# Kernel tuning notes

Measured on AMD Instinct MI355X. Metric: run time of the kernel, lower is better.

## Reference

```python
import jax, jax.numpy as jnp
import numpy as np

B, S, D, H = 2, 2048, 1024, 16
HD = D // H  # head_dim = 64
ROPE_BASE = 10000.0
NEG_MIN = jnp.finfo(jnp.float32).min


def _rope_cos_sin(seq_len, head_dim):
    inv_freq = 1.0 / (ROPE_BASE ** (jnp.arange(0, head_dim, 2, dtype=jnp.float32) / head_dim))
    t = jnp.arange(seq_len, dtype=jnp.float32)
    freqs = jnp.einsum('i,j->ij', t, inv_freq)           # [S, HD/2]
    emb = jnp.concatenate([freqs, freqs], axis=-1)        # [S, HD]
    return jnp.cos(emb), jnp.sin(emb)


def _rotate_half(x):
    x1, x2 = jnp.split(x, 2, axis=-1)
    return jnp.concatenate([-x2, x1], axis=-1)


def setup_inputs() -> dict:
    key = jax.random.key(0)
    ks = jax.random.split(key, 5)
    sc = 0.02
    hidden_states = jax.random.normal(ks[0], (B, S, D), dtype=jnp.float32)
    wq = jax.random.normal(ks[1], (D, D), dtype=jnp.float32) * sc
    wk = jax.random.normal(ks[2], (D, D), dtype=jnp.float32) * sc
    wv = jax.random.normal(ks[3], (D, D), dtype=jnp.float32) * sc
    wo = jax.random.normal(ks[4], (D, D), dtype=jnp.float32) * sc
    # additive causal mask [B,1,S,S]: 0 on/below diagonal, large negative above
    causal = jnp.tril(jnp.ones((S, S), dtype=jnp.bool_))
    attention_mask = jnp.where(causal, 0.0, NEG_MIN)[None, None, :, :].astype(jnp.float32)
    attention_mask = jnp.broadcast_to(attention_mask, (B, 1, S, S))
    position_ids = jnp.broadcast_to(jnp.arange(S, dtype=jnp.int32)[None, :], (B, S))
    return {"hidden_states": hidden_states, "attention_mask": attention_mask,
            "wq": wq, "wk": wk, "wv": wv, "wo": wo, "position_ids": position_ids}


def reference(hidden_states, attention_mask, wq, wk, wv, wo, position_ids):
    bsz, q_len, _ = hidden_states.shape

    def shape_heads(x):
        return x.reshape(bsz, q_len, H, HD).transpose(0, 2, 1, 3)  # [B,H,S,HD]

    q = shape_heads(hidden_states @ wq)
    k = shape_heads(hidden_states @ wk)
    v = shape_heads(hidden_states @ wv)

    cos, sin = _rope_cos_sin(q_len, HD)                   # [S, HD]
    cos = cos[position_ids][:, None, :, :]                # [B,1,S,HD]
    sin = sin[position_ids][:, None, :, :]
    q = q * cos + _rotate_half(q) * sin
    k = k * cos + _rotate_half(k) * sin

    scores = jnp.einsum('bhqd,bhkd->bhqk', q, k) / jnp.sqrt(jnp.float32(HD))
    scores = jnp.maximum(scores + attention_mask, NEG_MIN)
    attn = jax.nn.softmax(scores, axis=-1)
    out = jnp.einsum('bhqk,bhkd->bhqd', attn, v)          # [B,H,S,HD]
    out = out.transpose(0, 2, 1, 3).reshape(bsz, q_len, D)
    return out @ wo
```

## Files before the change

kernel.cpp:

```cpp
#include <hip/hip_runtime.h>
#include <hip/hip_bf16.h>

#define B_ 2
#define S_ 2048
#define D_ 1024
#define H_ 16
#define HD_ 64

typedef unsigned short u16;
typedef __attribute__((ext_vector_type(8))) short short8;
typedef __attribute__((ext_vector_type(4))) float f32x4;

#if __has_builtin(__builtin_amdgcn_exp2f)
#define EXP2F(x) __builtin_amdgcn_exp2f(x)
#else
#define EXP2F(x) exp2f(x)
#endif

__device__ __forceinline__ u16 f2bf(float f) {
  union { float f; unsigned u; } v; v.f = f;
  unsigned r = v.u + 0x7fffu + ((v.u >> 16) & 1u);
  return (u16)(r >> 16);
}
__device__ __forceinline__ unsigned pkbf(float a, float b) {
  union { __hip_bfloat162 h; unsigned u; } v;
  v.h = __float22bfloat162_rn(float2{a, b});
  return v.u;
}
__device__ __forceinline__ void gload_lds16(const u16* g, u16* l) {
  __builtin_amdgcn_global_load_lds((const __attribute__((address_space(1))) void*)g,
                                   (__attribute__((address_space(3))) void*)l, 16, 0, 0);
}

__global__ __launch_bounds__(256) void prep_kernel(const float* __restrict__ hs,
                                                   const float* __restrict__ W0,
                                                   const float* __restrict__ W1,
                                                   const float* __restrict__ W2,
                                                   const float* __restrict__ W3,
                                                   u16* __restrict__ Xb,
                                                   u16* __restrict__ WT) {
  __shared__ float T[64][65];
  if (blockIdx.z == 4) {
    const int base = (blockIdx.y * 16 + blockIdx.x) * 4096 + threadIdx.x;
#pragma unroll 4
    for (int i = 0; i < 16; ++i) {
      const int idx = base + i * 256;
      const float4 v = ((const float4*)hs)[idx];
      ushort4 o;
      o.x = f2bf(v.x); o.y = f2bf(v.y); o.z = f2bf(v.z); o.w = f2bf(v.w);
      ((ushort4*)Xb)[idx] = o;
    }
    return;
  }
  const float* Wz[4] = {W0, W1, W2, W3};
  const float* W = Wz[blockIdx.z];
  u16* dst = WT + (size_t)blockIdx.z * (1024 * 1024);
  const int nb = blockIdx.x * 64, kb = blockIdx.y * 64;
  const int t = threadIdx.x;
  const int r = t >> 2, c4 = (t & 3) * 16;
#pragma unroll
  for (int i = 0; i < 4; ++i) {
    float4 v = *(const float4*)&W[(kb + r) * D_ + nb + c4 + i * 4];
    T[r][c4 + i * 4 + 0] = v.x;
    T[r][c4 + i * 4 + 1] = v.y;
    T[r][c4 + i * 4 + 2] = v.z;
    T[r][c4 + i * 4 + 3] = v.w;
  }
  __syncthreads();
#pragma unroll
  for (int i = 0; i < 4; ++i) {
    ushort4 o;
    o.x = f2bf(T[c4 + i * 4 + 0][r]);
    o.y = f2bf(T[c4 + i * 4 + 1][r]);
    o.z = f2bf(T[c4 + i * 4 + 2][r]);
    o.w = f2bf(T[c4 + i * 4 + 3][r]);
    *(ushort4*)&dst[(nb + r) * D_ + kb + c4 + i * 4] = o;
  }
}

template <int BN, int MODE>
__global__ __launch_bounds__(256) void gemm_kernel(const u16* __restrict__ A,
                                                   const u16* __restrict__ BT,
                                                   float* __restrict__ out0,
                                                   u16* __restrict__ oQ,
                                                   u16* __restrict__ oK,
                                                   u16* __restrict__ oV,
                                                   const int* __restrict__ posarr) {
  constexpr int K = D_;
  constexpr int BK = 32;
  constexpr int NSTEP = K / BK;
  constexpr int NT = BN / 32;
  constexpr int NBR = (BN * BK) / 2048;
  constexpr int ABANK = 128 * BK;
  constexpr int BBANK = BN * BK;
  constexpr int BUFSZ = ABANK + BBANK;
  constexpr int EPIU = (MODE == 1) ? 128 * 136 : 0;
  constexpr int SMU = (3 * BUFSZ > EPIU) ? 3 * BUFSZ : EPIU;
  __shared__ u16 smem[SMU];

  const int t = threadIdx.x, lane = t & 63, w = t >> 6;
  const int l15 = lane & 15, quad = lane >> 4;
  const int flat = blockIdx.x;
  const int xcd = flat & 7, j = flat >> 3;
  const int m0 = ((xcd << 2) + (j & 3)) * 128;
  const int n0 = (j >> 2) * BN;
  const int wm = (w >> 1) * 64, wn = (w & 1) * (BN / 2);

  f32x4 acc[4][NT];
#pragma unroll
  for (int mt = 0; mt < 4; ++mt)
#pragma unroll
    for (int nt = 0; nt < NT; ++nt) acc[mt][nt] = (f32x4){0.f, 0.f, 0.f, 0.f};

  const u16* agp[2]; int adst[2];
  const u16* bgp[NBR]; int bdst[NBR];
#pragma unroll
  for (int jj = 0; jj < 2; ++jj) {
    const int slot = jj * 256 + w * 64 + lane;
    const int row = slot >> 2, c = slot & 3, q = c ^ ((row >> 1) & 3);
    agp[jj] = A + (size_t)(m0 + row) * K + q * 8;
    adst[jj] = (jj * 256 + w * 64) * 8;
  }
#pragma unroll
  for (int jj = 0; jj < NBR; ++jj) {
    const int slot = jj * 256 + w * 64 + lane;
    const int row = slot >> 2, c = slot & 3, q = c ^ ((row >> 1) & 3);
    bgp[jj] = BT + (size_t)(n0 + row) * K + q * 8;
    bdst[jj] = ABANK + (jj * 256 + w * 64) * 8;
  }

  auto stage = [&](int k0, int buf) {
    u16* base = smem + buf * BUFSZ;
#pragma unroll
    for (int jj = 0; jj < 2; ++jj) gload_lds16(agp[jj] + k0, base + adst[jj]);
#pragma unroll
    for (int jj = 0; jj < NBR; ++jj) gload_lds16(bgp[jj] + k0, base + bdst[jj]);
  };

  int afo[4], bfo[NT];
#pragma unroll
  for (int mt = 0; mt < 4; ++mt) {
    const int row = wm + mt * 16 + l15;
    afo[mt] = row * BK + (quad ^ ((row >> 1) & 3)) * 8;
  }
#pragma unroll
  for (int nt = 0; nt < NT; ++nt) {
    const int col = wn + nt * 16 + l15;
    bfo[nt] = ABANK + col * BK + (quad ^ ((col >> 1) & 3)) * 8;
  }

  auto compute = [&](int buf) {
    const u16* base = smem + buf * BUFSZ;
    short8 af[4], bf[NT];
#pragma unroll
    for (int mt = 0; mt < 4; ++mt) af[mt] = *(const short8*)&base[afo[mt]];
#pragma unroll
    for (int nt = 0; nt < NT; ++nt) bf[nt] = *(const short8*)&base[bfo[nt]];
#pragma unroll
    for (int mt = 0; mt < 4; ++mt)
#pragma unroll
      for (int nt = 0; nt < NT; ++nt)
        acc[mt][nt] = __builtin_amdgcn_mfma_f32_16x16x32_bf16(af[mt], bf[nt], acc[mt][nt], 0, 0, 0);
  };

  stage(0, 0);
  stage(BK, 1);
  int bc = 0, bs = 2;
#pragma unroll 1
  for (int it = 0; it < NSTEP - 2; ++it) {
    if constexpr (MODE == 1) asm volatile("s_waitcnt vmcnt(4)" ::: "memory");
    else                     asm volatile("s_waitcnt vmcnt(3)" ::: "memory");
    __builtin_amdgcn_s_barrier();
    __builtin_amdgcn_sched_barrier(0);
    stage((it + 2) * BK, bs);
    compute(bc);
    bc = bc == 2 ? 0 : bc + 1;
    bs = bs == 2 ? 0 : bs + 1;
  }
  if constexpr (MODE == 1) asm volatile("s_waitcnt vmcnt(4)" ::: "memory");
  else                     asm volatile("s_waitcnt vmcnt(3)" ::: "memory");
  __builtin_amdgcn_s_barrier();
  __builtin_amdgcn_sched_barrier(0);
  compute(bc);
  bc = bc == 2 ? 0 : bc + 1;
  asm volatile("s_waitcnt vmcnt(0)" ::: "memory");
  __builtin_amdgcn_s_barrier();
  __builtin_amdgcn_sched_barrier(0);
  compute(bc);

  if (MODE == 0) {
#pragma unroll
    for (int mt = 0; mt < 4; ++mt) {
      const int row0 = m0 + wm + mt * 16 + quad * 4;
#pragma unroll
      for (int nt = 0; nt < NT; ++nt) {
        const int col = n0 + wn + nt * 16 + l15;
#pragma unroll
        for (int r = 0; r < 4; ++r) out0[(size_t)(row0 + r) * 1024 + col] = acc[mt][nt][r];
      }
    }
  } else {
    const int widx = n0 >> 10;
    if (widx == 2) {
      __syncthreads();
      u16* Epi = smem;
#pragma unroll
      for (int nt = 0; nt < NT; ++nt) {
        const int col = wn + nt * 16 + l15;
#pragma unroll
        for (int mt = 0; mt < 4; ++mt) {
          const int row0 = wm + mt * 16 + quad * 4;
          uint2 pk;
          pk.x = pkbf(acc[mt][nt][0], acc[mt][nt][1]);
          pk.y = pkbf(acc[mt][nt][2], acc[mt][nt][3]);
          *(uint2*)&Epi[col * 136 + row0] = pk;
        }
      }
      __syncthreads();
      const int col = t >> 1, half = t & 1;
      const int cc = (n0 + col) & 1023;
      const int h = cc >> 6, d = cc & 63;
      const int bb = m0 >> 11;
      const int s0 = (m0 & (S_ - 1)) + half * 64;
      u16* gp = oV + ((((size_t)(bb * H_ + h) * HD_ + d)) << 11) + s0;
#pragma unroll
      for (int i = 0; i < 8; ++i)
        ((uint4*)gp)[i] = *(const uint4*)&Epi[col * 136 + half * 64 + i * 8];
    } else {
      u16* dst = (widx == 0) ? oQ : oK;
      const float scale = (widx == 0) ? 0.18033688011f : 1.0f;
      float invf[2];
      invf[0] = exp2f(-0.41524101186f * (float)l15);
      invf[1] = exp2f(-0.41524101186f * (float)(16 + l15));
      __syncthreads();
      u16* Epi = smem;
#pragma unroll
      for (int mt = 0; mt < 4; ++mt) {
        const int lrow0 = wm + mt * 16 + quad * 4;
#pragma unroll
        for (int r = 0; r < 4; ++r) {
          const int rw = m0 + lrow0 + r;
          const int b = rw >> 11, s = rw & (S_ - 1);
          const float pos = (float)posarr[b * S_ + s];
#pragma unroll
          for (int nt2 = 0; nt2 < 2; ++nt2) {
            float sn, c;
            __sincosf(pos * invf[nt2], &sn, &c);
            const float x1 = acc[mt][nt2][r], x2 = acc[mt][nt2 + 2][r];
            const int d = nt2 * 16 + l15;
            Epi[(lrow0 + r) * 136 + wn + d] = f2bf((x1 * c - x2 * sn) * scale);
            Epi[(lrow0 + r) * 136 + wn + d + 32] = f2bf((x2 * c + x1 * sn) * scale);
          }
        }
      }
      __syncthreads();
      const int bb = m0 >> 11, s0 = m0 & (S_ - 1);
      const int sl = t >> 1, d0 = (t & 1) * 32;
#pragma unroll
      for (int hh = 0; hh < 2; ++hh) {
        const int h = ((n0 + hh * 64) & 1023) >> 6;
        u16* gp = dst + (((size_t)(bb * H_ + h) * S_ + s0 + sl) << 6) + d0;
#pragma unroll
        for (int k2 = 0; k2 < 4; ++k2)
          ((uint4*)gp)[k2] = *(const uint4*)&Epi[sl * 136 + hh * 64 + d0 + k2 * 8];
      }
    }
  }
}

__global__ __launch_bounds__(256, 2) void attn_kernel(const u16* __restrict__ Q,
                                                      const u16* __restrict__ Kx,
                                                      const u16* __restrict__ Vt,
                                                      u16* __restrict__ AO) {
  __shared__ u16 Ks[2][2][512 * 8];
  __shared__ u16 Vs[2][2][512 * 8];
  __shared__ u16 Pw[4][128 * 8];
  const int t = threadIdx.x;
  const int lane = t & 63, w = t >> 6;
  const int l15 = lane & 15, quad = lane >> 4;
  const int idx = blockIdx.x;
  const int pr = (idx >> 3) & 15;
  const int bh = (idx & 7) | ((idx >> 7) << 3);
  const int qtA = pr, qtB = 31 - pr;
  const u16* qp = Q + bh * (S_ * HD_);
  const u16* kp = Kx + bh * (S_ * HD_);
  const u16* vp = Vt + bh * (HD_ * S_);
  const int wq16 = w * 16;
  const int q_loA = qtA * 64 + wq16;
  const int q_loB = qtB * 64 + wq16;

  int srow[2], sq[2];
#pragma unroll
  for (int jj = 0; jj < 2; ++jj) {
    int slot = w * 128 + jj * 64 + lane;
    srow[jj] = slot >> 3;
    sq[jj] = (slot & 7) ^ (srow[jj] & 7);
  }
  auto stageT = [&](int kt, int buf, int tt) {
#pragma unroll
    for (int jj = 0; jj < 2; ++jj)
      gload_lds16(kp + (size_t)(kt * 64 + srow[jj]) * 64 + sq[jj] * 8,
                  &Ks[buf][tt][(w * 128 + jj * 64) * 8]);
#pragma unroll
    for (int jj = 0; jj < 2; ++jj)
      gload_lds16(vp + (size_t)srow[jj] * S_ + kt * 64 + sq[jj] * 8,
                  &Vs[buf][tt][(w * 128 + jj * 64) * 8]);
  };
  auto stageGroup = [&](int g, int buf, int ktmax) {
    const int kt0 = g * 2;
    stageT(kt0, buf, 0);
    if (kt0 + 1 <= ktmax) stageT(kt0 + 1, buf, 1);
  };

  short8 qfA[2], qfB[2];
#pragma unroll
  for (int kc = 0; kc < 2; ++kc) {
    qfA[kc] = *(const short8*)&qp[(q_loA + l15) * HD_ + kc * 32 + quad * 8];
    qfB[kc] = *(const short8*)&qp[(q_loB + l15) * HD_ + kc * 32 + quad * 8];
  }

  f32x4 oA[4], oB[4];
  float mA = -INFINITY, lA = 0.f, mB = -INFINITY, lB = 0.f;
#pragma unroll
  for (int i = 0; i < 4; ++i) {
    oA[i] = (f32x4){0.f, 0.f, 0.f, 0.f};
    oB[i] = (f32x4){0.f, 0.f, 0.f, 0.f};
  }

  auto chainStep = [&](bool diag, const short8* qf, const short8* kf, const short8* vf,
                       f32x4* o, float& m_, float& l_) {
    f32x4 sa[4];
#pragma unroll
    for (int i = 0; i < 4; ++i) sa[i] = (f32x4){0.f, 0.f, 0.f, 0.f};
#pragma unroll
    for (int kc = 0; kc < 2; ++kc)
#pragma unroll
      for (int nt = 0; nt < 4; ++nt)
        sa[nt] = __builtin_amdgcn_mfma_f32_16x16x32_bf16(kf[kc * 4 + nt], qf[kc], sa[nt], 0, 0, 0);
    if (diag) {
#pragma unroll
      for (int nt = 0; nt < 4; ++nt)
#pragma unroll
        for (int r = 0; r < 4; ++r)
          if (nt * 16 + quad * 4 + r > wq16 + l15) sa[nt][r] = -INFINITY;
    }
    float mx = -INFINITY;
#pragma unroll
    for (int nt = 0; nt < 4; ++nt)
#pragma unroll
      for (int r = 0; r < 4; ++r) mx = fmaxf(mx, sa[nt][r]);
    mx = fmaxf(mx, __shfl_xor(mx, 16));
    mx = fmaxf(mx, __shfl_xor(mx, 32));
    const float mn = fmaxf(m_, mx);
    const float alpha = EXP2F(m_ - mn);
    m_ = mn;
    float p[16];
    float sum = 0.f;
#pragma unroll
    for (int nt = 0; nt < 4; ++nt)
#pragma unroll
      for (int r = 0; r < 4; ++r) {
        const float pe = EXP2F(sa[nt][r] - mn);
        p[nt * 4 + r] = pe;
        sum += pe;
      }
    sum += __shfl_xor(sum, 16);
    sum += __shfl_xor(sum, 32);
    l_ = l_ * alpha + sum;
#pragma unroll
    for (int dt = 0; dt < 4; ++dt)
#pragma unroll
      for (int r = 0; r < 4; ++r) o[dt][r] *= alpha;
#pragma unroll
    for (int nt = 0; nt < 4; ++nt) {
      const int q = nt * 2 + (quad >> 1);
      uint2 pk;
      pk.x = pkbf(p[nt * 4 + 0], p[nt * 4 + 1]);
      pk.y = pkbf(p[nt * 4 + 2], p[nt * 4 + 3]);
      *(uint2*)&Pw[w][(l15 * 8 + (q ^ (l15 & 7))) * 8 + (quad & 1) * 4] = pk;
    }
#pragma unroll
    for (int kc = 0; kc < 2; ++kc) {
      short8 pf = *(const short8*)&Pw[w][(l15 * 8 + (((kc * 4) + quad) ^ (l15 & 7))) * 8];
#pragma unroll
      for (int dt = 0; dt < 4; ++dt)
        o[dt] = __builtin_amdgcn_mfma_f32_16x16x32_bf16(vf[dt * 2 + kc], pf, o[dt], 0, 0, 0);
    }
  };

  auto loadFrags = [&](int buf, int tt, short8* kf, short8* vf) {
#pragma unroll
    for (int kc = 0; kc < 2; ++kc)
#pragma unroll
      for (int nt = 0; nt < 4; ++nt) {
        const int row = nt * 16 + l15;
        kf[kc * 4 + nt] =
            *(const short8*)&Ks[buf][tt][(row * 8 + ((kc * 4 + quad) ^ (row & 7))) * 8];
      }
#pragma unroll
    for (int dt = 0; dt < 4; ++dt)
#pragma unroll
      for (int kc = 0; kc < 2; ++kc) {
        const int row = dt * 16 + l15;
        vf[dt * 2 + kc] =
            *(const short8*)&Vs[buf][tt][(row * 8 + ((kc * 4 + quad) ^ (row & 7))) * 8];
      }
  };

  const int ktmax = qtB;
  const int ngroups = (ktmax + 2) >> 1;
  short8 kf[8], vf[8];
  stageGroup(0, 0, ktmax);
#pragma unroll 1
  for (int g = 0; g < ngroups; ++g) {
    __syncthreads();
    if (g + 1 < ngroups) stageGroup(g + 1, (g + 1) & 1, ktmax);
    const int buf = g & 1;
    const int kt0 = 2 * g;
    loadFrags(buf, 0, kf, vf);
    chainStep(kt0 == qtB, qfB, kf, vf, oB, mB, lB);
    if (kt0 <= qtA) chainStep(kt0 == qtA, qfA, kf, vf, oA, mA, lA);
    if (kt0 + 1 <= ktmax) {
      loadFrags(buf, 1, kf, vf);
      chainStep(kt0 + 1 == qtB, qfB, kf, vf, oB, mB, lB);
      if (kt0 + 1 <= qtA) chainStep(kt0 + 1 == qtA, qfA, kf, vf, oA, mA, lA);
    }
  }

  const int b = bh >> 4, h = bh & 15;
  const float liA = 1.0f / lA, liB = 1.0f / lB;
  const size_t baseA = ((size_t)(b * S_ + q_loA + l15)) * D_ + h * HD_;
  const size_t baseB = ((size_t)(b * S_ + q_loB + l15)) * D_ + h * HD_;
#pragma unroll
  for (int dt = 0; dt < 4; ++dt)
#pragma unroll
    for (int rr = 0; rr < 2; ++rr) {
      *(unsigned*)&AO[baseA + dt * 16 + quad * 4 + rr * 2] =
          pkbf(oA[dt][rr * 2] * liA, oA[dt][rr * 2 + 1] * liA);
      *(unsigned*)&AO[baseB + dt * 16 + quad * 4 + rr * 2] =
          pkbf(oB[dt][rr * 2] * liB, oB[dt][rr * 2 + 1] * liB);
    }
}

extern "C" void kernel_launch(void* const* d_in, const int* in_sizes, int n_in,
                              void* d_out, int out_size, void* d_ws, size_t ws_size,
                              hipStream_t stream) {
  const float* hs = (const float*)d_in[0];
  const float* wq = (const float*)d_in[2];
  const float* wk = (const float*)d_in[3];
  const float* wv = (const float*)d_in[4];
  const float* wo = (const float*)d_in[5];
  const int* pos = (const int*)d_in[6];
  float* out = (float*)d_out;

  char* ws = (char*)d_ws;
  const size_t MB = (size_t)1 << 20;
  u16* Xb = (u16*)(ws);
  u16* WT = (u16*)(ws + 8 * MB);
  u16* Qh = (u16*)(ws + 16 * MB);
  u16* Kh = (u16*)(ws + 24 * MB);
  u16* Vt = (u16*)(ws + 32 * MB);
  u16* AO = (u16*)(ws + 40 * MB);

  prep_kernel<<<dim3(16, 16, 5), 256, 0, stream>>>(hs, wq, wk, wv, wo, Xb, WT);

  gemm_kernel<128, 1><<<768, 256, 0, stream>>>(Xb, WT, nullptr, Qh, Kh, Vt, pos);

  attn_kernel<<<512, 256, 0, stream>>>(Qh, Kh, Vt, AO);

  gemm_kernel<64, 0><<<512, 256, 0, stream>>>(AO, WT + 3 * 1024 * 1024, out,
                                              nullptr, nullptr, nullptr, nullptr);
}
```

Measured before the change: 201.1 us.

## Split attention blocks to one query tile each with row sums via MFMA

Each attention block used to process a paired short and long query tile. It now handles a single query tile, so the grid doubles to 1024 blocks, LDS staging is single-tile double-buffered, and launch bounds allow 4 blocks per CU for higher occupancy. The softmax row sum is now accumulated with an extra MFMA against a ones vector instead of shuffles. Rescaling is skipped when the running max does not change, and setprio hints are placed around the MFMA sections. In exchange, each K/V tile is no longer reused by two query tiles, which raises global and LDS traffic per unit of work, and an interleaved long/short tile ordering is relied on to balance the causal workload.

After: 222.7 us. +10.7%, slower.

```diff
diff --git a/kernel.cpp b/kernel.cpp
--- a/kernel.cpp
+++ b/kernel.cpp
@@ -268,26 +268,26 @@
   }
 }
 
-__global__ __launch_bounds__(256, 2) void attn_kernel(const u16* __restrict__ Q,
+__global__ __launch_bounds__(256, 4) void attn_kernel(const u16* __restrict__ Q,
                                                       const u16* __restrict__ Kx,
                                                       const u16* __restrict__ Vt,
                                                       u16* __restrict__ AO) {
-  __shared__ u16 Ks[2][2][512 * 8];
-  __shared__ u16 Vs[2][2][512 * 8];
+  __shared__ u16 Ks[2][512 * 8];
+  __shared__ u16 Vs[2][512 * 8];
   __shared__ u16 Pw[4][128 * 8];
   const int t = threadIdx.x;
   const int lane = t & 63, w = t >> 6;
   const int l15 = lane & 15, quad = lane >> 4;
   const int idx = blockIdx.x;
-  const int pr = (idx >> 3) & 15;
-  const int bh = (idx & 7) | ((idx >> 7) << 3);
-  const int qtA = pr, qtB = 31 - pr;
+  const int r = idx >> 3;
+  const int j = r & 31;
+  const int qt = (j & 1) ? (j >> 1) : (31 - (j >> 1));
+  const int bh = (idx & 7) | ((r >> 5) << 3);
   const u16* qp = Q + bh * (S_ * HD_);
   const u16* kp = Kx + bh * (S_ * HD_);
   const u16* vp = Vt + bh * (HD_ * S_);
   const int wq16 = w * 16;
-  const int q_loA = qtA * 64 + wq16;
-  const int q_loB = qtB * 64 + wq16;
+  const int q_lo = qt * 64 + wq16;
 
   int srow[2], sq[2];
 #pragma unroll
@@ -296,81 +296,96 @@
     srow[jj] = slot >> 3;
     sq[jj] = (slot & 7) ^ (srow[jj] & 7);
   }
-  auto stageT = [&](int kt, int buf, int tt) {
+  auto stage = [&](int kt, int buf) {
 #pragma unroll
     for (int jj = 0; jj < 2; ++jj)
       gload_lds16(kp + (size_t)(kt * 64 + srow[jj]) * 64 + sq[jj] * 8,
-                  &Ks[buf][tt][(w * 128 + jj * 64) * 8]);
+                  &Ks[buf][(w * 128 + jj * 64) * 8]);
 #pragma unroll
     for (int jj = 0; jj < 2; ++jj)
       gload_lds16(vp + (size_t)srow[jj] * S_ + kt * 64 + sq[jj] * 8,
-                  &Vs[buf][tt][(w * 128 + jj * 64) * 8]);
+                  &Vs[buf][(w * 128 + jj * 64) * 8]);
   };
-  auto stageGroup = [&](int g, int buf, int ktmax) {
-    const int kt0 = g * 2;
-    stageT(kt0, buf, 0);
-    if (kt0 + 1 <= ktmax) stageT(kt0 + 1, buf, 1);
-  };
-
-  short8 qfA[2], qfB[2];
-#pragma unroll
-  for (int kc = 0; kc < 2; ++kc) {
-    qfA[kc] = *(const short8*)&qp[(q_loA + l15) * HD_ + kc * 32 + quad * 8];
-    qfB[kc] = *(const short8*)&qp[(q_loB + l15) * HD_ + kc * 32 + quad * 8];
-  }
-
-  f32x4 oA[4], oB[4];
-  float mA = -INFINITY, lA = 0.f, mB = -INFINITY, lB = 0.f;
-#pragma unroll
-  for (int i = 0; i < 4; ++i) {
-    oA[i] = (f32x4){0.f, 0.f, 0.f, 0.f};
-    oB[i] = (f32x4){0.f, 0.f, 0.f, 0.f};
-  }
-
-  auto chainStep = [&](bool diag, const short8* qf, const short8* kf, const short8* vf,
-                       f32x4* o, float& m_, float& l_) {
+
+  short8 qf[2];
+#pragma unroll
+  for (int kc = 0; kc < 2; ++kc)
+    qf[kc] = *(const short8*)&qp[(q_lo + l15) * HD_ + kc * 32 + quad * 8];
+
+  f32x4 o[4];
+  f32x4 lsum = (f32x4){0.f, 0.f, 0.f, 0.f};
+  float m_ = -INFINITY;
+#pragma unroll
+  for (int i = 0; i < 4; ++i) o[i] = (f32x4){0.f, 0.f, 0.f, 0.f};
+  const short8 ones = {0x3F80, 0x3F80, 0x3F80, 0x3F80, 0x3F80, 0x3F80, 0x3F80, 0x3F80};
+
+  stage(0, 0);
+#pragma unroll 1
+  for (int kt = 0; kt <= qt; ++kt) {
+    __syncthreads();
+    if (kt < qt) stage(kt + 1, (kt + 1) & 1);
+    const int buf = kt & 1;
+
+    short8 kf[8];
+#pragma unroll
+    for (int kc = 0; kc < 2; ++kc)
+#pragma unroll
+      for (int nt = 0; nt < 4; ++nt) {
+        const int row = nt * 16 + l15;
+        kf[kc * 4 + nt] =
+            *(const short8*)&Ks[buf][(row * 8 + ((kc * 4 + quad) ^ (row & 7))) * 8];
+      }
     f32x4 sa[4];
 #pragma unroll
     for (int i = 0; i < 4; ++i) sa[i] = (f32x4){0.f, 0.f, 0.f, 0.f};
+    __builtin_amdgcn_s_setprio(1);
 #pragma unroll
     for (int kc = 0; kc < 2; ++kc)
 #pragma unroll
       for (int nt = 0; nt < 4; ++nt)
         sa[nt] = __builtin_amdgcn_mfma_f32_16x16x32_bf16(kf[kc * 4 + nt], qf[kc], sa[nt], 0, 0, 0);
-    if (diag) {
+    __builtin_amdgcn_s_setprio(0);
+
+    short8 vf[8];
+#pragma unroll
+    for (int dt = 0; dt < 4; ++dt)
+#pragma unroll
+      for (int kc = 0; kc < 2; ++kc) {
+        const int row = dt * 16 + l15;
+        vf[dt * 2 + kc] =
+            *(const short8*)&Vs[buf][(row * 8 + ((kc * 4 + quad) ^ (row & 7))) * 8];
+      }
+
+    if (kt == qt) {
 #pragma unroll
       for (int nt = 0; nt < 4; ++nt)
 #pragma unroll
-        for (int r = 0; r < 4; ++r)
-          if (nt * 16 + quad * 4 + r > wq16 + l15) sa[nt][r] = -INFINITY;
-    }
-    float mx = -INFINITY;
+        for (int rr = 0; rr < 4; ++rr)
+          if (nt * 16 + quad * 4 + rr > wq16 + l15) sa[nt][rr] = -INFINITY;
+    }
+    float mq[4];
 #pragma unroll
     for (int nt = 0; nt < 4; ++nt)
-#pragma unroll
-      for (int r = 0; r < 4; ++r) mx = fmaxf(mx, sa[nt][r]);
+      mq[nt] = fmaxf(fmaxf(sa[nt][0], sa[nt][1]), fmaxf(sa[nt][2], sa[nt][3]));
+    float mx = fmaxf(fmaxf(mq[0], mq[1]), fmaxf(mq[2], mq[3]));
     mx = fmaxf(mx, __shfl_xor(mx, 16));
     mx = fmaxf(mx, __shfl_xor(mx, 32));
-    const float mn = fmaxf(m_, mx);
-    const float alpha = EXP2F(m_ - mn);
-    m_ = mn;
+    if (!__all(mx <= m_)) {
+      const float mn = fmaxf(m_, mx);
+      const float alpha = EXP2F(m_ - mn);
+      m_ = mn;
+#pragma unroll
+      for (int dt = 0; dt < 4; ++dt)
+#pragma unroll
+        for (int rr = 0; rr < 4; ++rr) o[dt][rr] *= alpha;
+#pragma unroll
+      for (int rr = 0; rr < 4; ++rr) lsum[rr] *= alpha;
+    }
     float p[16];
-    float sum = 0.f;
 #pragma unroll
     for (int nt = 0; nt < 4; ++nt)
 #pragma unroll
-      for (int r = 0; r < 4; ++r) {
-        const float pe = EXP2F(sa[nt][r] - mn);
-        p[nt * 4 + r] = pe;
-        sum += pe;
-      }
-    sum += __shfl_xor(sum, 16);
-    sum += __shfl_xor(sum, 32);
-    l_ = l_ * alpha + sum;
-#pragma unroll
-    for (int dt = 0; dt < 4; ++dt)
-#pragma unroll
-      for (int r = 0; r < 4; ++r) o[dt][r] *= alpha;
+      for (int rr = 0; rr < 4; ++rr) p[nt * 4 + rr] = EXP2F(sa[nt][rr] - m_);
 #pragma unroll
     for (int nt = 0; nt < 4; ++nt) {
       const int q = nt * 2 + (quad >> 1);
@@ -379,67 +394,27 @@
       pk.y = pkbf(p[nt * 4 + 2], p[nt * 4 + 3]);
       *(uint2*)&Pw[w][(l15 * 8 + (q ^ (l15 & 7))) * 8 + (quad & 1) * 4] = pk;
     }
+    __builtin_amdgcn_s_setprio(1);
 #pragma unroll
     for (int kc = 0; kc < 2; ++kc) {
       short8 pf = *(const short8*)&Pw[w][(l15 * 8 + (((kc * 4) + quad) ^ (l15 & 7))) * 8];
 #pragma unroll
       for (int dt = 0; dt < 4; ++dt)
         o[dt] = __builtin_amdgcn_mfma_f32_16x16x32_bf16(vf[dt * 2 + kc], pf, o[dt], 0, 0, 0);
-    }
-  };
-
-  auto loadFrags = [&](int buf, int tt, short8* kf, short8* vf) {
-#pragma unroll
-    for (int kc = 0; kc < 2; ++kc)
-#pragma unroll
-      for (int nt = 0; nt < 4; ++nt) {
-        const int row = nt * 16 + l15;
-        kf[kc * 4 + nt] =
-            *(const short8*)&Ks[buf][tt][(row * 8 + ((kc * 4 + quad) ^ (row & 7))) * 8];
-      }
-#pragma unroll
-    for (int dt = 0; dt < 4; ++dt)
-#pragma unroll
-      for (int kc = 0; kc < 2; ++kc) {
-        const int row = dt * 16 + l15;
-        vf[dt * 2 + kc] =
-            *(const short8*)&Vs[buf][tt][(row * 8 + ((kc * 4 + quad) ^ (row & 7))) * 8];
-      }
-  };
-
-  const int ktmax = qtB;
-  const int ngroups = (ktmax + 2) >> 1;
-  short8 kf[8], vf[8];
-  stageGroup(0, 0, ktmax);
-#pragma unroll 1
-  for (int g = 0; g < ngroups; ++g) {
-    __syncthreads();
-    if (g + 1 < ngroups) stageGroup(g + 1, (g + 1) & 1, ktmax);
-    const int buf = g & 1;
-    const int kt0 = 2 * g;
-    loadFrags(buf, 0, kf, vf);
-    chainStep(kt0 == qtB, qfB, kf, vf, oB, mB, lB);
-    if (kt0 <= qtA) chainStep(kt0 == qtA, qfA, kf, vf, oA, mA, lA);
-    if (kt0 + 1 <= ktmax) {
-      loadFrags(buf, 1, kf, vf);
-      chainStep(kt0 + 1 == qtB, qfB, kf, vf, oB, mB, lB);
-      if (kt0 + 1 <= qtA) chainStep(kt0 + 1 == qtA, qfA, kf, vf, oA, mA, lA);
-    }
+      lsum = __builtin_amdgcn_mfma_f32_16x16x32_bf16(ones, pf, lsum, 0, 0, 0);
+    }
+    __builtin_amdgcn_s_setprio(0);
   }
 
   const int b = bh >> 4, h = bh & 15;
-  const float liA = 1.0f / lA, liB = 1.0f / lB;
-  const size_t baseA = ((size_t)(b * S_ + q_loA + l15)) * D_ + h * HD_;
-  const size_t baseB = ((size_t)(b * S_ + q_loB + l15)) * D_ + h * HD_;
+  const float li = 1.0f / lsum[0];
+  const size_t base = ((size_t)(b * S_ + q_lo + l15)) * D_ + h * HD_;
 #pragma unroll
   for (int dt = 0; dt < 4; ++dt)
 #pragma unroll
-    for (int rr = 0; rr < 2; ++rr) {
-      *(unsigned*)&AO[baseA + dt * 16 + quad * 4 + rr * 2] =
-          pkbf(oA[dt][rr * 2] * liA, oA[dt][rr * 2 + 1] * liA);
-      *(unsigned*)&AO[baseB + dt * 16 + quad * 4 + rr * 2] =
-          pkbf(oB[dt][rr * 2] * liB, oB[dt][rr * 2 + 1] * liB);
-    }
+    for (int rr = 0; rr < 2; ++rr)
+      *(unsigned*)&AO[base + dt * 16 + quad * 4 + rr * 2] =
+          pkbf(o[dt][rr * 2] * li, o[dt][rr * 2 + 1] * li);
 }
 
 extern "C" void kernel_launch(void* const* d_in, const int* in_sizes, int n_in,
@@ -466,7 +441,7 @@
 
   gemm_kernel<128, 1><<<768, 256, 0, stream>>>(Xb, WT, nullptr, Qh, Kh, Vt, pos);
 
-  attn_kernel<<<512, 256, 0, stream>>>(Qh, Kh, Vt, AO);
+  attn_kernel<<<1024, 256, 0, stream>>>(Qh, Kh, Vt, AO);
 
   gemm_kernel<64, 0><<<512, 256, 0, stream>>>(AO, WT + 3 * 1024 * 1024, out,
                                               nullptr, nullptr, nullptr, nullptr);
```

## Compute softmax row sums via MFMA, skip rescale when max unchanged, add setprio

Applied to the files above, without the earlier changes.

Replaces the per-lane row-sum reduction with an extra MFMA against a ones vector, so the row sum comes from the same bf16 P values used for the PV product. The alpha rescale of the accumulators is skipped when no lane's running max increases. The QK and PV MFMA blocks are wrapped in s_setprio, and the P scratch buffer is split per chain (A/B) so the two chains can overlap in LDS. It removes VALU work and shuffles from the softmax path but adds two MFMAs per step and a wave-wide vote branch.

Measured after the change: 203.4 us. About the same (+1.1%).

```diff
diff --git a/kernel.cpp b/kernel.cpp
--- a/kernel.cpp
+++ b/kernel.cpp
@@ -274,7 +274,7 @@
                                                       u16* __restrict__ AO) {
   __shared__ u16 Ks[2][2][512 * 8];
   __shared__ u16 Vs[2][2][512 * 8];
-  __shared__ u16 Pw[4][128 * 8];
+  __shared__ u16 Pw[4][2][128 * 8];
   const int t = threadIdx.x;
   const int lane = t & 63, w = t >> 6;
   const int l15 = lane & 15, quad = lane >> 4;
@@ -320,23 +320,27 @@
   }
 
   f32x4 oA[4], oB[4];
-  float mA = -INFINITY, lA = 0.f, mB = -INFINITY, lB = 0.f;
+  f32x4 lsA = (f32x4){0.f, 0.f, 0.f, 0.f}, lsB = (f32x4){0.f, 0.f, 0.f, 0.f};
+  float mA = -INFINITY, mB = -INFINITY;
 #pragma unroll
   for (int i = 0; i < 4; ++i) {
     oA[i] = (f32x4){0.f, 0.f, 0.f, 0.f};
     oB[i] = (f32x4){0.f, 0.f, 0.f, 0.f};
   }
+  const short8 ones = {0x3F80, 0x3F80, 0x3F80, 0x3F80, 0x3F80, 0x3F80, 0x3F80, 0x3F80};
 
   auto chainStep = [&](bool diag, const short8* qf, const short8* kf, const short8* vf,
-                       f32x4* o, float& m_, float& l_) {
+                       f32x4* o, float& m_, f32x4& ls, u16* pwb) {
     f32x4 sa[4];
 #pragma unroll
     for (int i = 0; i < 4; ++i) sa[i] = (f32x4){0.f, 0.f, 0.f, 0.f};
+    __builtin_amdgcn_s_setprio(1);
 #pragma unroll
     for (int kc = 0; kc < 2; ++kc)
 #pragma unroll
       for (int nt = 0; nt < 4; ++nt)
         sa[nt] = __builtin_amdgcn_mfma_f32_16x16x32_bf16(kf[kc * 4 + nt], qf[kc], sa[nt], 0, 0, 0);
+    __builtin_amdgcn_s_setprio(0);
     if (diag) {
 #pragma unroll
       for (int nt = 0; nt < 4; ++nt)
@@ -344,48 +348,41 @@
         for (int r = 0; r < 4; ++r)
           if (nt * 16 + quad * 4 + r > wq16 + l15) sa[nt][r] = -INFINITY;
     }
-    float mx = -INFINITY;
+    float mq[4];
 #pragma unroll
     for (int nt = 0; nt < 4; ++nt)
-#pragma unroll
-      for (int r = 0; r < 4; ++r) mx = fmaxf(mx, sa[nt][r]);
+      mq[nt] = fmaxf(fmaxf(sa[nt][0], sa[nt][1]), fmaxf(sa[nt][2], sa[nt][3]));
+    float mx = fmaxf(fmaxf(mq[0], mq[1]), fmaxf(mq[2], mq[3]));
     mx = fmaxf(mx, __shfl_xor(mx, 16));
     mx = fmaxf(mx, __shfl_xor(mx, 32));
-    const float mn = fmaxf(m_, mx);
-    const float alpha = EXP2F(m_ - mn);
-    m_ = mn;
-    float p[16];
-    float sum = 0.f;
-#pragma unroll
-    for (int nt = 0; nt < 4; ++nt)
-#pragma unroll
-      for (int r = 0; r < 4; ++r) {
-        const float pe = EXP2F(sa[nt][r] - mn);
-        p[nt * 4 + r] = pe;
-        sum += pe;
-      }
-    sum += __shfl_xor(sum, 16);
-    sum += __shfl_xor(sum, 32);
-    l_ = l_ * alpha + sum;
-#pragma unroll
-    for (int dt = 0; dt < 4; ++dt)
-#pragma unroll
-      for (int r = 0; r < 4; ++r) o[dt][r] *= alpha;
+    if (!__all(mx <= m_)) {
+      const float mn = fmaxf(m_, mx);
+      const float alpha = EXP2F(m_ - mn);
+      m_ = mn;
+#pragma unroll
+      for (int dt = 0; dt < 4; ++dt)
+#pragma unroll
+        for (int r = 0; r < 4; ++r) o[dt][r] *= alpha;
+      ls *= alpha;
+    }
 #pragma unroll
     for (int nt = 0; nt < 4; ++nt) {
       const int q = nt * 2 + (quad >> 1);
       uint2 pk;
-      pk.x = pkbf(p[nt * 4 + 0], p[nt * 4 + 1]);
-      pk.y = pkbf(p[nt * 4 + 2], p[nt * 4 + 3]);
-      *(uint2*)&Pw[w][(l15 * 8 + (q ^ (l15 & 7))) * 8 + (quad & 1) * 4] = pk;
-    }
+      pk.x = pkbf(EXP2F(sa[nt][0] - m_), EXP2F(sa[nt][1] - m_));
+      pk.y = pkbf(EXP2F(sa[nt][2] - m_), EXP2F(sa[nt][3] - m_));
+      *(uint2*)&pwb[(l15 * 8 + (q ^ (l15 & 7))) * 8 + (quad & 1) * 4] = pk;
+    }
+    __builtin_amdgcn_s_setprio(1);
 #pragma unroll
     for (int kc = 0; kc < 2; ++kc) {
-      short8 pf = *(const short8*)&Pw[w][(l15 * 8 + (((kc * 4) + quad) ^ (l15 & 7))) * 8];
+      short8 pf = *(const short8*)&pwb[(l15 * 8 + (((kc * 4) + quad) ^ (l15 & 7))) * 8];
 #pragma unroll
       for (int dt = 0; dt < 4; ++dt)
         o[dt] = __builtin_amdgcn_mfma_f32_16x16x32_bf16(vf[dt * 2 + kc], pf, o[dt], 0, 0, 0);
-    }
+      ls = __builtin_amdgcn_mfma_f32_16x16x32_bf16(ones, pf, ls, 0, 0, 0);
+    }
+    __builtin_amdgcn_s_setprio(0);
   };
 
   auto loadFrags = [&](int buf, int tt, short8* kf, short8* vf) {
@@ -418,17 +415,17 @@
     const int buf = g & 1;
     const int kt0 = 2 * g;
     loadFrags(buf, 0, kf, vf);
-    chainStep(kt0 == qtB, qfB, kf, vf, oB, mB, lB);
-    if (kt0 <= qtA) chainStep(kt0 == qtA, qfA, kf, vf, oA, mA, lA);
+    chainStep(kt0 == qtB, qfB, kf, vf, oB, mB, lsB, &Pw[w][1][0]);
+    if (kt0 <= qtA) chainStep(kt0 == qtA, qfA, kf, vf, oA, mA, lsA, &Pw[w][0][0]);
     if (kt0 + 1 <= ktmax) {
       loadFrags(buf, 1, kf, vf);
-      chainStep(kt0 + 1 == qtB, qfB, kf, vf, oB, mB, lB);
-      if (kt0 + 1 <= qtA) chainStep(kt0 + 1 == qtA, qfA, kf, vf, oA, mA, lA);
+      chainStep(kt0 + 1 == qtB, qfB, kf, vf, oB, mB, lsB, &Pw[w][1][0]);
+      if (kt0 + 1 <= qtA) chainStep(kt0 + 1 == qtA, qfA, kf, vf, oA, mA, lsA, &Pw[w][0][0]);
     }
   }
 
   const int b = bh >> 4, h = bh & 15;
-  const float liA = 1.0f / lA, liB = 1.0f / lB;
+  const float liA = 1.0f / lsA[0], liB = 1.0f / lsB[0];
   const size_t baseA = ((size_t)(b * S_ + q_loA + l15)) * D_ + h * HD_;
   const size_t baseB = ((size_t)(b * S_ + q_loB + l15)) * D_ + h * HD_;
 #pragma unroll
```

## Restructure attention kernel to 32x32 MFMA with per-wave chain split

Applied to the files above, without the earlier changes.

The attention kernel switches from 16x16x32 to 32x32x16 bf16 MFMA tiles. Each pair of waves now owns one of the two query tiles (A or B), with each wave covering 32 query rows, instead of every wave processing both tiles with 16 rows each. It also adds a third XOR term to the LDS swizzle and skips the online-softmax rescale when no row max increases. Two waves now have much less work than the other two because of the causal imbalance between tile A and tile B, which risks idle waves in exchange for fewer, larger MFMAs and less fragment reloading.

Result: slower. 218.5 us (+8.6%).

```diff
diff --git a/kernel.cpp b/kernel.cpp
--- a/kernel.cpp
+++ b/kernel.cpp
@@ -10,6 +10,7 @@
 typedef unsigned short u16;
 typedef __attribute__((ext_vector_type(8))) short short8;
 typedef __attribute__((ext_vector_type(4))) float f32x4;
+typedef __attribute__((ext_vector_type(16))) float f32x16;
 
 #if __has_builtin(__builtin_amdgcn_exp2f)
 #define EXP2F(x) __builtin_amdgcn_exp2f(x)
@@ -274,27 +275,28 @@
                                                       u16* __restrict__ AO) {
   __shared__ u16 Ks[2][2][512 * 8];
   __shared__ u16 Vs[2][2][512 * 8];
-  __shared__ u16 Pw[4][128 * 8];
+  __shared__ u16 Pq[4][2048];
   const int t = threadIdx.x;
   const int lane = t & 63, w = t >> 6;
-  const int l15 = lane & 15, quad = lane >> 4;
+  const int q5 = lane & 31, hi = lane >> 5;
   const int idx = blockIdx.x;
   const int pr = (idx >> 3) & 15;
   const int bh = (idx & 7) | ((idx >> 7) << 3);
   const int qtA = pr, qtB = 31 - pr;
+  const int chain = w >> 1, half = w & 1;
+  const int my_qt = chain ? qtB : qtA;
+  const int q_row_local = half * 32 + q5;
+  const int q_global = my_qt * 64 + q_row_local;
   const u16* qp = Q + bh * (S_ * HD_);
   const u16* kp = Kx + bh * (S_ * HD_);
   const u16* vp = Vt + bh * (HD_ * S_);
-  const int wq16 = w * 16;
-  const int q_loA = qtA * 64 + wq16;
-  const int q_loB = qtB * 64 + wq16;
 
   int srow[2], sq[2];
 #pragma unroll
   for (int jj = 0; jj < 2; ++jj) {
     int slot = w * 128 + jj * 64 + lane;
     srow[jj] = slot >> 3;
-    sq[jj] = (slot & 7) ^ (srow[jj] & 7);
+    sq[jj] = (slot & 7) ^ (srow[jj] & 7) ^ ((srow[jj] >> 3) & 3);
   }
   auto stageT = [&](int kt, int buf, int tt) {
 #pragma unroll
@@ -312,104 +314,99 @@
     if (kt0 + 1 <= ktmax) stageT(kt0 + 1, buf, 1);
   };
 
-  short8 qfA[2], qfB[2];
-#pragma unroll
-  for (int kc = 0; kc < 2; ++kc) {
-    qfA[kc] = *(const short8*)&qp[(q_loA + l15) * HD_ + kc * 32 + quad * 8];
-    qfB[kc] = *(const short8*)&qp[(q_loB + l15) * HD_ + kc * 32 + quad * 8];
-  }
-
-  f32x4 oA[4], oB[4];
-  float mA = -INFINITY, lA = 0.f, mB = -INFINITY, lB = 0.f;
-#pragma unroll
-  for (int i = 0; i < 4; ++i) {
-    oA[i] = (f32x4){0.f, 0.f, 0.f, 0.f};
-    oB[i] = (f32x4){0.f, 0.f, 0.f, 0.f};
-  }
-
-  auto chainStep = [&](bool diag, const short8* qf, const short8* kf, const short8* vf,
-                       f32x4* o, float& m_, float& l_) {
-    f32x4 sa[4];
-#pragma unroll
-    for (int i = 0; i < 4; ++i) sa[i] = (f32x4){0.f, 0.f, 0.f, 0.f};
-#pragma unroll
-    for (int kc = 0; kc < 2; ++kc)
-#pragma unroll
-      for (int nt = 0; nt < 4; ++nt)
-        sa[nt] = __builtin_amdgcn_mfma_f32_16x16x32_bf16(kf[kc * 4 + nt], qf[kc], sa[nt], 0, 0, 0);
-    if (diag) {
-#pragma unroll
-      for (int nt = 0; nt < 4; ++nt)
-#pragma unroll
-        for (int r = 0; r < 4; ++r)
-          if (nt * 16 + quad * 4 + r > wq16 + l15) sa[nt][r] = -INFINITY;
+  short8 qf[4];
+#pragma unroll
+  for (int ks = 0; ks < 4; ++ks)
+    qf[ks] = *(const short8*)&qp[(size_t)q_global * HD_ + ks * 16 + hi * 8];
+
+  f32x16 o0, o1;
+  float m_ = -INFINITY, l_ = 0.f;
+#pragma unroll
+  for (int i = 0; i < 16; ++i) { o0[i] = 0.f; o1[i] = 0.f; }
+
+  auto fusedTile = [&](int buf, int tt, int kt) {
+    f32x16 sa0, sa1;
+#pragma unroll
+    for (int i = 0; i < 16; ++i) { sa0[i] = 0.f; sa1[i] = 0.f; }
+#pragma unroll
+    for (int ks = 0; ks < 4; ++ks) {
+      const int c8 = ks * 2 + hi;
+      {
+        const int r64 = q5;
+        short8 kf = *(const short8*)&Ks[buf][tt][(r64 * 8 + (c8 ^ (r64 & 7) ^ ((r64 >> 3) & 3))) * 8];
+        sa0 = __builtin_amdgcn_mfma_f32_32x32x16_bf16(kf, qf[ks], sa0, 0, 0, 0);
+      }
+      {
+        const int r64 = 32 + q5;
+        short8 kf = *(const short8*)&Ks[buf][tt][(r64 * 8 + (c8 ^ (r64 & 7) ^ ((r64 >> 3) & 3))) * 8];
+        sa1 = __builtin_amdgcn_mfma_f32_32x32x16_bf16(kf, qf[ks], sa1, 0, 0, 0);
+      }
+    }
+    if (kt == my_qt) {
+#pragma unroll
+      for (int jj = 0; jj < 16; ++jj) {
+        const int kl = (jj & 3) + 8 * (jj >> 2) + 4 * hi;
+        if (kl > q_row_local) sa0[jj] = -INFINITY;
+        if (kl + 32 > q_row_local) sa1[jj] = -INFINITY;
+      }
     }
     float mx = -INFINITY;
 #pragma unroll
-    for (int nt = 0; nt < 4; ++nt)
-#pragma unroll
-      for (int r = 0; r < 4; ++r) mx = fmaxf(mx, sa[nt][r]);
-    mx = fmaxf(mx, __shfl_xor(mx, 16));
+    for (int jj = 0; jj < 16; ++jj) mx = fmaxf(mx, fmaxf(sa0[jj], sa1[jj]));
     mx = fmaxf(mx, __shfl_xor(mx, 32));
-    const float mn = fmaxf(m_, mx);
-    const float alpha = EXP2F(m_ - mn);
-    m_ = mn;
-    float p[16];
+    if (!__all(mx <= m_)) {
+      const float mn = fmaxf(m_, mx);
+      const float alpha = EXP2F(m_ - mn);
+      m_ = mn;
+#pragma unroll
+      for (int i = 0; i < 16; ++i) { o0[i] *= alpha; o1[i] *= alpha; }
+      l_ *= alpha;
+    }
     float sum = 0.f;
 #pragma unroll
-    for (int nt = 0; nt < 4; ++nt)
-#pragma unroll
-      for (int r = 0; r < 4; ++r) {
-        const float pe = EXP2F(sa[nt][r] - mn);
-        p[nt * 4 + r] = pe;
-        sum += pe;
-      }
-    sum += __shfl_xor(sum, 16);
+    for (int rt = 0; rt < 2; ++rt) {
+#pragma unroll
+      for (int jc = 0; jc < 4; ++jc) {
+        float pe[4];
+#pragma unroll
+        for (int r = 0; r < 4; ++r) {
+          const float v = (rt == 0) ? sa0[jc * 4 + r] : sa1[jc * 4 + r];
+          pe[r] = EXP2F(v - m_);
+          sum += pe[r];
+        }
+        uint2 pk;
+        pk.x = pkbf(pe[0], pe[1]);
+        pk.y = pkbf(pe[2], pe[3]);
+        const int ch = rt * 4 + jc;
+        *(uint2*)&Pq[w][q5 * 64 + ((ch ^ (q5 & 7) ^ ((q5 >> 3) & 3)) * 8) + hi * 4] = pk;
+      }
+    }
     sum += __shfl_xor(sum, 32);
-    l_ = l_ * alpha + sum;
-#pragma unroll
-    for (int dt = 0; dt < 4; ++dt)
-#pragma unroll
-      for (int r = 0; r < 4; ++r) o[dt][r] *= alpha;
-#pragma unroll
-    for (int nt = 0; nt < 4; ++nt) {
-      const int q = nt * 2 + (quad >> 1);
-      uint2 pk;
-      pk.x = pkbf(p[nt * 4 + 0], p[nt * 4 + 1]);
-      pk.y = pkbf(p[nt * 4 + 2], p[nt * 4 + 3]);
-      *(uint2*)&Pw[w][(l15 * 8 + (q ^ (l15 & 7))) * 8 + (quad & 1) * 4] = pk;
-    }
-#pragma unroll
-    for (int kc = 0; kc < 2; ++kc) {
-      short8 pf = *(const short8*)&Pw[w][(l15 * 8 + (((kc * 4) + quad) ^ (l15 & 7))) * 8];
-#pragma unroll
-      for (int dt = 0; dt < 4; ++dt)
-        o[dt] = __builtin_amdgcn_mfma_f32_16x16x32_bf16(vf[dt * 2 + kc], pf, o[dt], 0, 0, 0);
-    }
-  };
-
-  auto loadFrags = [&](int buf, int tt, short8* kf, short8* vf) {
-#pragma unroll
-    for (int kc = 0; kc < 2; ++kc)
-#pragma unroll
-      for (int nt = 0; nt < 4; ++nt) {
-        const int row = nt * 16 + l15;
-        kf[kc * 4 + nt] =
-            *(const short8*)&Ks[buf][tt][(row * 8 + ((kc * 4 + quad) ^ (row & 7))) * 8];
-      }
-#pragma unroll
-    for (int dt = 0; dt < 4; ++dt)
-#pragma unroll
-      for (int kc = 0; kc < 2; ++kc) {
-        const int row = dt * 16 + l15;
-        vf[dt * 2 + kc] =
-            *(const short8*)&Vs[buf][tt][(row * 8 + ((kc * 4 + quad) ^ (row & 7))) * 8];
-      }
+    l_ += sum;
+    short8 pf[4];
+#pragma unroll
+    for (int ks = 0; ks < 4; ++ks) {
+      const int ch = ks * 2 + hi;
+      pf[ks] = *(const short8*)&Pq[w][q5 * 64 + ((ch ^ (q5 & 7) ^ ((q5 >> 3) & 3)) * 8)];
+    }
+#pragma unroll
+    for (int ks = 0; ks < 4; ++ks) {
+      const int c8 = ks * 2 + hi;
+      {
+        const int r64 = q5;
+        short8 vf = *(const short8*)&Vs[buf][tt][(r64 * 8 + (c8 ^ (r64 & 7) ^ ((r64 >> 3) & 3))) * 8];
+        o0 = __builtin_amdgcn_mfma_f32_32x32x16_bf16(vf, pf[ks], o0, 0, 0, 0);
+      }
+      {
+        const int r64 = 32 + q5;
+        short8 vf = *(const short8*)&Vs[buf][tt][(r64 * 8 + (c8 ^ (r64 & 7) ^ ((r64 >> 3) & 3))) * 8];
+        o1 = __builtin_amdgcn_mfma_f32_32x32x16_bf16(vf, pf[ks], o1, 0, 0, 0);
+      }
+    }
   };
 
   const int ktmax = qtB;
   const int ngroups = (ktmax + 2) >> 1;
-  short8 kf[8], vf[8];
   stageGroup(0, 0, ktmax);
 #pragma unroll 1
   for (int g = 0; g < ngroups; ++g) {
@@ -417,29 +414,29 @@
     if (g + 1 < ngroups) stageGroup(g + 1, (g + 1) & 1, ktmax);
     const int buf = g & 1;
     const int kt0 = 2 * g;
-    loadFrags(buf, 0, kf, vf);
-    chainStep(kt0 == qtB, qfB, kf, vf, oB, mB, lB);
-    if (kt0 <= qtA) chainStep(kt0 == qtA, qfA, kf, vf, oA, mA, lA);
-    if (kt0 + 1 <= ktmax) {
-      loadFrags(buf, 1, kf, vf);
-      chainStep(kt0 + 1 == qtB, qfB, kf, vf, oB, mB, lB);
-      if (kt0 + 1 <= qtA) chainStep(kt0 + 1 == qtA, qfA, kf, vf, oA, mA, lA);
-    }
+    if (kt0 <= my_qt) fusedTile(buf, 0, kt0);
+    if (kt0 + 1 <= ktmax && kt0 + 1 <= my_qt) fusedTile(buf, 1, kt0 + 1);
   }
 
   const int b = bh >> 4, h = bh & 15;
-  const float liA = 1.0f / lA, liB = 1.0f / lB;
-  const size_t baseA = ((size_t)(b * S_ + q_loA + l15)) * D_ + h * HD_;
-  const size_t baseB = ((size_t)(b * S_ + q_loB + l15)) * D_ + h * HD_;
-#pragma unroll
-  for (int dt = 0; dt < 4; ++dt)
-#pragma unroll
-    for (int rr = 0; rr < 2; ++rr) {
-      *(unsigned*)&AO[baseA + dt * 16 + quad * 4 + rr * 2] =
-          pkbf(oA[dt][rr * 2] * liA, oA[dt][rr * 2 + 1] * liA);
-      *(unsigned*)&AO[baseB + dt * 16 + quad * 4 + rr * 2] =
-          pkbf(oB[dt][rr * 2] * liB, oB[dt][rr * 2 + 1] * liB);
-    }
+  const float li = 1.0f / l_;
+  const size_t base = ((size_t)(b * S_ + q_global)) * D_ + h * HD_;
+#pragma unroll
+  for (int dt = 0; dt < 2; ++dt) {
+#pragma unroll
+    for (int jc = 0; jc < 4; ++jc) {
+      const int d0 = dt * 32 + jc * 8 + hi * 4;
+      uint2 pk;
+      if (dt == 0) {
+        pk.x = pkbf(o0[jc * 4 + 0] * li, o0[jc * 4 + 1] * li);
+        pk.y = pkbf(o0[jc * 4 + 2] * li, o0[jc * 4 + 3] * li);
+      } else {
+        pk.x = pkbf(o1[jc * 4 + 0] * li, o1[jc * 4 + 1] * li);
+        pk.y = pkbf(o1[jc * 4 + 2] * li, o1[jc * 4 + 3] * li);
+      }
+      *(uint2*)&AO[base + d0] = pk;
+    }
+  }
 }
 
 extern "C" void kernel_launch(void* const* d_in, const int* in_sizes, int n_in,
```
